# Performance work log

Hardware: AMD Instinct MI355X
Metric: run time of the kernel (lower is better)

## Reference

```python
import jax, jax.numpy as jnp
import numpy as np
import itertools

ZOOM = 2.0  # zoom_factor per init_kwargs


def _interpn_linear(vol, locs):
    """vol: [*vol_shape, C]; locs: list of nb_dims float arrays of shape new_shape."""
    nb = len(locs)
    C = vol.shape[-1]
    max_loc = [vol.shape[d] - 1 for d in range(nb)]
    clipped = [jnp.clip(locs[d], 0.0, max_loc[d]) for d in range(nb)]
    loc0 = [jnp.clip(jnp.floor(locs[d]), 0.0, max_loc[d]) for d in range(nb)]
    loc1 = [jnp.clip(loc0[d] + 1.0, 0.0, max_loc[d]) for d in range(nb)]
    i0 = [x.astype(jnp.int32) for x in loc0]
    i1 = [x.astype(jnp.int32) for x in loc1]
    diff1 = [loc1[d] - clipped[d] for d in range(nb)]  # weight paired with corner 0
    diff0 = [1.0 - diff1[d] for d in range(nb)]        # weight paired with corner 1
    idxs = [i0, i1]
    wts = [diff1, diff0]
    volf = vol.reshape(-1, C)
    # column-major-style flattening per sub2ind: k = cumprod(reversed vol_shape)
    k = np.cumprod(np.array(vol.shape[:-1])[::-1])
    out = jnp.zeros(locs[0].shape + (C,), dtype=vol.dtype)
    for c in itertools.product([0, 1], repeat=nb):  # 2^nb corners (fixed, small)
        subs = [idxs[c[d]][d] for d in range(nb)]
        flat = subs[-1]
        for i, v in enumerate(subs[:-1][::-1]):
            flat = flat + v * int(k[i])
        val = volf[flat]  # gather -> [*new_shape, C]
        w = wts[c[0]][0]
        for d in range(1, nb):
            w = w * wts[c[d]][d]
        out = out + w[..., None] * val
    return out


def _resize_one(vol):
    """vol: [D,H,W,C] -> [2D,2H,2W,C] via linear interp at loc = grid/zoom."""
    nb = vol.ndim - 1
    new_shape = tuple(int(vol.shape[d] * ZOOM) for d in range(nb))
    grids = jnp.meshgrid(*[jnp.arange(n, dtype=jnp.float32) for n in new_shape],
                         indexing='ij')
    locs = [g / ZOOM for g in grids]  # grid + offset, offset = grid/zoom - grid
    return _interpn_linear(vol, locs)


def setup_inputs() -> dict:
    key = jax.random.key(0)
    vol = jax.random.normal(key, (2, 96, 96, 96, 2), dtype=jnp.float32)
    return {"vol": vol}


def reference(vol):
    return jax.vmap(_resize_one)(vol)  # [B, 192, 192, 192, 2]
```

## Files before the change

### kernel.cpp

```cpp
#include <hip/hip_runtime.h>

#define NIN 96
#define NOUT 192
#define BATCH 2
#define NVOX (NIN * NIN * NIN)

__device__ __forceinline__ float2 f2_add(float2 a, float2 b) {
    return make_float2(a.x + b.x, a.y + b.y);
}
__device__ __forceinline__ float2 f2_scale(float2 a, float s) {
    return make_float2(a.x * s, a.y * s);
}

__global__ __launch_bounds__(256) void resize_zoom2_kernel(
        const float* __restrict__ in, float* __restrict__ out) {
    int idx = blockIdx.x * blockDim.x + threadIdx.x;
    int x = idx % NIN;
    int t = idx / NIN;
    int y = t % NIN;
    t /= NIN;
    int z = t % NIN;
    int b = t / NIN;

    int x1 = min(x + 1, NIN - 1);
    int y1 = min(y + 1, NIN - 1);
    int z1 = min(z + 1, NIN - 1);

    const float* vb = in + (size_t)b * (NVOX * 2);

    size_t r00 = (((size_t)z  * NIN + y ) * NIN) * 2;
    size_t r01 = (((size_t)z  * NIN + y1) * NIN) * 2;
    size_t r10 = (((size_t)z1 * NIN + y ) * NIN) * 2;
    size_t r11 = (((size_t)z1 * NIN + y1) * NIN) * 2;

    float2 v000 = *(const float2*)(vb + r00 + (size_t)x  * 2);
    float2 v001 = *(const float2*)(vb + r00 + (size_t)x1 * 2);
    float2 v010 = *(const float2*)(vb + r01 + (size_t)x  * 2);
    float2 v011 = *(const float2*)(vb + r01 + (size_t)x1 * 2);
    float2 v100 = *(const float2*)(vb + r10 + (size_t)x  * 2);
    float2 v101 = *(const float2*)(vb + r10 + (size_t)x1 * 2);
    float2 v110 = *(const float2*)(vb + r11 + (size_t)x  * 2);
    float2 v111 = *(const float2*)(vb + r11 + (size_t)x1 * 2);

    float2 e_ee = v000;
    float2 o_ee = f2_scale(f2_add(v000, v001), 0.5f);
    float2 e_oe = f2_scale(f2_add(v000, v010), 0.5f);
    float2 o_oe = f2_scale(f2_add(f2_add(v000, v001), f2_add(v010, v011)), 0.25f);

    float2 e_ez = f2_scale(f2_add(v000, v100), 0.5f);
    float2 o_ez = f2_scale(f2_add(f2_add(v000, v001), f2_add(v100, v101)), 0.25f);
    float2 e_oz = f2_scale(f2_add(f2_add(v000, v010), f2_add(v100, v110)), 0.25f);
    float2 o_oz = f2_scale(
        f2_add(f2_add(f2_add(v000, v001), f2_add(v010, v011)),
               f2_add(f2_add(v100, v101), f2_add(v110, v111))), 0.125f);

    float* ob = out + (size_t)b * ((size_t)NOUT * NOUT * NOUT * 2);
    int xo = 2 * x, yo = 2 * y, zo = 2 * z;
    size_t q = (((size_t)zo * NOUT + yo) * NOUT + xo) * 2;
    const size_t rowStride   = (size_t)NOUT * 2;
    const size_t planeStride = (size_t)NOUT * NOUT * 2;

    *(float4*)(ob + q)                            = make_float4(e_ee.x, e_ee.y, o_ee.x, o_ee.y);
    *(float4*)(ob + q + rowStride)                = make_float4(e_oe.x, e_oe.y, o_oe.x, o_oe.y);
    *(float4*)(ob + q + planeStride)              = make_float4(e_ez.x, e_ez.y, o_ez.x, o_ez.y);
    *(float4*)(ob + q + planeStride + rowStride)  = make_float4(e_oz.x, e_oz.y, o_oz.x, o_oz.y);
}

extern "C" void kernel_launch(void* const* d_in, const int* in_sizes, int n_in,
                              void* d_out, int out_size, void* d_ws, size_t ws_size,
                              hipStream_t stream) {
    const float* in = (const float*)d_in[0];
    float* out = (float*)d_out;
    const int total = BATCH * NVOX;
    const int block = 256;
    const int grid = total / block;
    resize_zoom2_kernel<<<grid, block, 0, stream>>>(in, out);
}
```

Baseline: 129.5 us.

## Stage input tiles with halo in shared memory and emit contiguous output rows

Each block loads a 5x5 by 97 input tile (4x4 z,y brick of full x rows plus a one-voxel halo) into LDS. Threads then produce full output rows of float4 values in order, which replaces the old pattern of four strided float4 stores per thread with contiguous, coalesced row writes. It also removes redundant global reads of the eight neighbours. The costs are a __syncthreads, LDS pressure of about 19KB per block, and a smaller grid of 1152 blocks.

```diff
diff --git a/kernel.cpp b/kernel.cpp
--- a/kernel.cpp
+++ b/kernel.cpp
@@ -1,69 +1,63 @@
 #include <hip/hip_runtime.h>
 
-#define NIN 96
-#define NOUT 192
-#define BATCH 2
-#define NVOX (NIN * NIN * NIN)
+constexpr int NIN  = 96;
+constexpr int NOUT = 192;
+constexpr int TZ = 4, TY = 4;
+constexpr int HZ = TZ + 1, HY = TY + 1, HX = NIN + 1;
+constexpr int NT = NIN / TZ;
 
-__device__ __forceinline__ float2 f2_add(float2 a, float2 b) {
-    return make_float2(a.x + b.x, a.y + b.y);
-}
-__device__ __forceinline__ float2 f2_scale(float2 a, float s) {
-    return make_float2(a.x * s, a.y * s);
-}
+__global__ __launch_bounds__(256) void resize_zoom2_tiled(
+        const float* __restrict__ in, float* __restrict__ out) {
+    __shared__ float2 S[HZ * HY * HX];
 
-__global__ __launch_bounds__(256) void resize_zoom2_kernel(
-        const float* __restrict__ in, float* __restrict__ out) {
-    int idx = blockIdx.x * blockDim.x + threadIdx.x;
-    int x = idx % NIN;
-    int t = idx / NIN;
-    int y = t % NIN;
-    t /= NIN;
-    int z = t % NIN;
-    int b = t / NIN;
+    int bid = blockIdx.x;
+    int yt = bid % NT;
+    int t  = bid / NT;
+    int zt = t % NT;
+    int b  = t / NT;
+    int z0 = zt * TZ, y0 = yt * TY;
 
-    int x1 = min(x + 1, NIN - 1);
-    int y1 = min(y + 1, NIN - 1);
-    int z1 = min(z + 1, NIN - 1);
+    const float2* vin = (const float2*)in + (size_t)b * ((size_t)NIN * NIN * NIN);
 
-    const float* vb = in + (size_t)b * (NVOX * 2);
+    for (int i = threadIdx.x; i < HZ * HY * HX; i += 256) {
+        int xx = i % HX;
+        int r  = i / HX;
+        int dy = r % HY;
+        int dz = r / HY;
+        int zi = min(z0 + dz, NIN - 1);
+        int yi = min(y0 + dy, NIN - 1);
+        int xi = min(xx, NIN - 1);
+        S[i] = vin[((size_t)zi * NIN + yi) * NIN + xi];
+    }
+    __syncthreads();
 
-    size_t r00 = (((size_t)z  * NIN + y ) * NIN) * 2;
-    size_t r01 = (((size_t)z  * NIN + y1) * NIN) * 2;
-    size_t r10 = (((size_t)z1 * NIN + y ) * NIN) * 2;
-    size_t r11 = (((size_t)z1 * NIN + y1) * NIN) * 2;
+    float4* vout = (float4*)out;
+    int Zb = 2 * z0, Yb = 2 * y0;
 
-    float2 v000 = *(const float2*)(vb + r00 + (size_t)x  * 2);
-    float2 v001 = *(const float2*)(vb + r00 + (size_t)x1 * 2);
-    float2 v010 = *(const float2*)(vb + r01 + (size_t)x  * 2);
-    float2 v011 = *(const float2*)(vb + r01 + (size_t)x1 * 2);
-    float2 v100 = *(const float2*)(vb + r10 + (size_t)x  * 2);
-    float2 v101 = *(const float2*)(vb + r10 + (size_t)x1 * 2);
-    float2 v110 = *(const float2*)(vb + r11 + (size_t)x  * 2);
-    float2 v111 = *(const float2*)(vb + r11 + (size_t)x1 * 2);
-
-    float2 e_ee = v000;
-    float2 o_ee = f2_scale(f2_add(v000, v001), 0.5f);
-    float2 e_oe = f2_scale(f2_add(v000, v010), 0.5f);
-    float2 o_oe = f2_scale(f2_add(f2_add(v000, v001), f2_add(v010, v011)), 0.25f);
-
-    float2 e_ez = f2_scale(f2_add(v000, v100), 0.5f);
-    float2 o_ez = f2_scale(f2_add(f2_add(v000, v001), f2_add(v100, v101)), 0.25f);
-    float2 e_oz = f2_scale(f2_add(f2_add(v000, v010), f2_add(v100, v110)), 0.25f);
-    float2 o_oz = f2_scale(
-        f2_add(f2_add(f2_add(v000, v001), f2_add(v010, v011)),
-               f2_add(f2_add(v100, v101), f2_add(v110, v111))), 0.125f);
-
-    float* ob = out + (size_t)b * ((size_t)NOUT * NOUT * NOUT * 2);
-    int xo = 2 * x, yo = 2 * y, zo = 2 * z;
-    size_t q = (((size_t)zo * NOUT + yo) * NOUT + xo) * 2;
-    const size_t rowStride   = (size_t)NOUT * 2;
-    const size_t planeStride = (size_t)NOUT * NOUT * 2;
-
-    *(float4*)(ob + q)                            = make_float4(e_ee.x, e_ee.y, o_ee.x, o_ee.y);
-    *(float4*)(ob + q + rowStride)                = make_float4(e_oe.x, e_oe.y, o_oe.x, o_oe.y);
-    *(float4*)(ob + q + planeStride)              = make_float4(e_ez.x, e_ez.y, o_ez.x, o_ez.y);
-    *(float4*)(ob + q + planeStride + rowStride)  = make_float4(e_oz.x, e_oz.y, o_oz.x, o_oz.y);
+    #pragma unroll 4
+    for (int k = 0; k < 24; ++k) {
+        int j  = threadIdx.x + k * 256;
+        int xp = j % NIN;
+        int r  = j / NIN;
+        int yo = r & 7;
+        int zo = r >> 3;
+        int zA = zo >> 1, zB = zA + (zo & 1);
+        int yA = yo >> 1, yB = yA + (yo & 1);
+        const float2* rowAA = S + (zA * HY + yA) * HX;
+        const float2* rowAB = S + (zA * HY + yB) * HX;
+        const float2* rowBA = S + (zB * HY + yA) * HX;
+        const float2* rowBB = S + (zB * HY + yB) * HX;
+        float2 a0 = rowAA[xp],     a1 = rowAB[xp],     a2 = rowBA[xp],     a3 = rowBB[xp];
+        float2 c0 = rowAA[xp + 1], c1 = rowAB[xp + 1], c2 = rowBA[xp + 1], c3 = rowBB[xp + 1];
+        float sex = a0.x + a1.x + a2.x + a3.x;
+        float sey = a0.y + a1.y + a2.y + a3.y;
+        float sox = c0.x + c1.x + c2.x + c3.x;
+        float soy = c0.y + c1.y + c2.y + c3.y;
+        float4 v = make_float4(0.25f * sex, 0.25f * sey,
+                               0.125f * (sex + sox), 0.125f * (sey + soy));
+        size_t o4 = (((size_t)(b * NOUT + (Zb + zo))) * NOUT + (Yb + yo)) * (NOUT / 2) + xp;
+        vout[o4] = v;
+    }
 }
 
 extern "C" void kernel_launch(void* const* d_in, const int* in_sizes, int n_in,
@@ -71,8 +65,6 @@
                               hipStream_t stream) {
     const float* in = (const float*)d_in[0];
     float* out = (float*)d_out;
-    const int total = BATCH * NVOX;
-    const int block = 256;
-    const int grid = total / block;
-    resize_zoom2_kernel<<<grid, block, 0, stream>>>(in, out);
+    const int grid = 2 * NT * NT;
+    resize_zoom2_tiled<<<grid, 256, 0, stream>>>(in, out);
 }
```

Measured after the change: 124.7 us. -3.7%, faster.
